# Kernel tuning notes

Hardware: AMD Instinct MI355X
Metric: run time of the kernel (lower is better)

The kernel has to match this reference:

```python
import jax, jax.numpy as jnp
import numpy as np

NUM_NODES = 100000
HIDDEN = 128
OFFSET = 2  # GNNEmbedding.OFFSET


def gcn_conv(x, src, dst, W, b, n):
    # GCNConv: D^{-1/2} (A + I) D^{-1/2} X W + b, with self-loops added
    loops = jnp.arange(n)
    s = jnp.concatenate([src, loops])
    d = jnp.concatenate([dst, loops])
    deg = jax.ops.segment_sum(jnp.ones(s.shape, x.dtype), d, num_segments=n)
    dinv = jax.lax.rsqrt(jnp.maximum(deg, 1e-12))
    norm = dinv[s] * dinv[d]          # [E+n]
    msg = x[s] * norm[:, None]        # [E+n, H]  dominant memory traffic
    agg = jax.ops.segment_sum(msg, d, num_segments=n)
    return agg @ W + b


def setup_inputs():
    key = jax.random.key(0)
    ks = jax.random.split(key, 8)
    E = 1_600_000
    B, S = 16, 2048
    src = jax.random.randint(ks[0], (E,), 0, NUM_NODES)
    dst = jax.random.randint(ks[1], (E,), 0, NUM_NODES)
    ei = jnp.stack([src, dst])
    seq = jax.random.randint(ks[2], (B, S), 0, NUM_NODES)
    specials = jax.random.randint(ks[3], (B, S), -2, 20)
    seq = jnp.where(specials < 0, specials, seq)
    emb = jax.random.normal(ks[4], (NUM_NODES + 2, HIDDEN), jnp.float32) * 0.02
    lim = 1.0 / np.sqrt(HIDDEN)
    W0 = jax.random.uniform(ks[5], (HIDDEN, HIDDEN), jnp.float32, -lim, lim)
    W1 = jax.random.uniform(ks[6], (HIDDEN, HIDDEN), jnp.float32, -lim, lim)
    b0 = jnp.zeros((HIDDEN,), jnp.float32)
    b1 = jnp.zeros((HIDDEN,), jnp.float32)
    return {"emb": emb, "W0": W0, "b0": b0, "W1": W1, "b1": b1,
            "ei": ei, "seq": seq}


def reference(emb, W0, b0, W1, b1, ei, seq):
    src, dst = ei[0], ei[1]
    x = emb[:NUM_NODES]                               # embedding(arange(num_nodes))
    h = jax.nn.relu(gcn_conv(x, src, dst, W0, b0, NUM_NODES))
    z = gcn_conv(h, src, dst, W1, b1, NUM_NODES)      # no act on last GCN layer
    nodes = seq >= 0
    node_idx = jnp.where(nodes, seq, 0)
    spec_idx = jnp.where(nodes, 0, seq + OFFSET + NUM_NODES)
    # embs[nodes] = z[seq[nodes]]; embs[~nodes] = emb[seq+OFFSET+num_nodes]
    embs = jnp.where(nodes[..., None], z[node_idx], emb[spec_idx])
    return embs
```

## Files before the change

kernel.cpp:

```cpp
#include <hip/hip_runtime.h>

#define HDIM 128
#define OFF_SPECIAL 2
#define BSTRIDE 48

typedef __attribute__((ext_vector_type(8))) short bf16x8;
typedef __attribute__((ext_vector_type(4))) float f32x4;

__device__ __forceinline__ float bf2f(unsigned short u) {
    union { unsigned int i; float f; } v;
    v.i = ((unsigned int)u) << 16;
    return v.f;
}
__device__ __forceinline__ unsigned short f2bf(float f) {
    union { float f; unsigned int i; } v;
    v.f = f;
    unsigned int x = v.i;
    x += 0x7FFFu + ((x >> 16) & 1u);
    return (unsigned short)(x >> 16);
}

#define FILL_BLOCKS 1024
#define CAST_BLOCKS 512
#define FLAG_BLOCKS 16

__global__ void k_fill_cast(const int* __restrict__ src, const int* __restrict__ dst,
                            int E, int* __restrict__ cnt, int* __restrict__ adjB,
                            int partN,
                            const float* __restrict__ emb,
                            unsigned short* __restrict__ embbf, int n4,
                            const int* __restrict__ seqp, int P,
                            unsigned char* __restrict__ flag) {
    int tid = threadIdx.x;
    if (blockIdx.x < FILL_BLOCKS) {
        int part = blockIdx.x & 7;
        int blk  = blockIdx.x >> 3;
        int lo = part * partN;
        int hi = lo + partN;
        int nGroups = (E + 3) >> 2;
        int stride = (FILL_BLOCKS >> 3) * 256;
        for (int g = blk * 256 + tid; g < nGroups; g += stride) {
            int4 d4 = ((const int4*)dst)[g];
            int4 s4 = ((const int4*)src)[g];
            int e0 = g * 4;
            int dd[4] = {d4.x, d4.y, d4.z, d4.w};
            int ss[4] = {s4.x, s4.y, s4.z, s4.w};
#pragma unroll
            for (int j = 0; j < 4; ++j) {
                int d = dd[j];
                if (e0 + j < E && d >= lo && d < hi) {
                    int slot = atomicAdd(&cnt[d], 1);
                    if (slot < BSTRIDE) adjB[d * BSTRIDE + slot] = ss[j];
                }
            }
        }
    } else if (blockIdx.x < FILL_BLOCKS + CAST_BLOCKS) {
        int i0 = (blockIdx.x - FILL_BLOCKS) * 256 + tid;
        for (int i = i0; i < n4; i += CAST_BLOCKS * 256) {
            float4 v = ((const float4*)emb)[i];
            ushort4 o;
            o.x = f2bf(v.x); o.y = f2bf(v.y); o.z = f2bf(v.z); o.w = f2bf(v.w);
            ((ushort4*)embbf)[i] = o;
        }
    } else {
        int i0 = (blockIdx.x - FILL_BLOCKS - CAST_BLOCKS) * 256 + tid;
        for (int p = i0; p < P; p += FLAG_BLOCKS * 256) {
            int sv = seqp[p];
            if (sv >= 0) flag[sv] = 1;
        }
    }
}

__global__ void k_dinv(const int* __restrict__ cnt, float* __restrict__ dinv, int N) {
    int i = blockIdx.x * blockDim.x + threadIdx.x;
    if (i < N) dinv[i] = rsqrtf((float)cnt[i] + 1.0f);
}

template <int SPARSE>
__global__ __launch_bounds__(256, 8) void k_pull(
        const unsigned short* __restrict__ x, const int* __restrict__ cnt,
        const int* __restrict__ adjB, const float* __restrict__ dinv,
        unsigned short* __restrict__ agg, int N,
        const unsigned char* __restrict__ flag) {
    int row = blockIdx.x * 4 + (threadIdx.x >> 6);
    if (row >= N) return;
    if (SPARSE && !flag[row]) return;
    int lane = threadIdx.x & 63;
    int d = cnt[row];
    if (d > BSTRIDE) d = BSTRIDE;
    const int* nbr = adjB + row * BSTRIDE;
    float dr = dinv[row];
    unsigned int cix = 2u * (unsigned int)lane;

    float ax, ay;
    {
        float sc = dr * dr;
        unsigned int u = *(const unsigned int*)(x + (size_t)(unsigned)row * HDIM + cix);
        ax = bf2f((unsigned short)u) * sc;
        ay = bf2f((unsigned short)(u >> 16)) * sc;
    }
    int t = 0;
    for (; t + 8 <= d; t += 8) {
        int4 q0 = *(const int4*)(nbr + t);
        int4 q1 = *(const int4*)(nbr + t + 4);
        int s[8] = {q0.x, q0.y, q0.z, q0.w, q1.x, q1.y, q1.z, q1.w};
        float nr[8];
        unsigned int u[8];
#pragma unroll
        for (int i = 0; i < 8; ++i) {
            nr[i] = dinv[s[i]] * dr;
            u[i] = *(const unsigned int*)(x + (size_t)(unsigned)s[i] * HDIM + cix);
        }
#pragma unroll
        for (int i = 0; i < 8; ++i) {
            ax = fmaf(bf2f((unsigned short)u[i]), nr[i], ax);
            ay = fmaf(bf2f((unsigned short)(u[i] >> 16)), nr[i], ay);
        }
    }
    if (t + 4 <= d) {
        int4 q0 = *(const int4*)(nbr + t);
        int s[4] = {q0.x, q0.y, q0.z, q0.w};
        float nr[4];
        unsigned int u[4];
#pragma unroll
        for (int i = 0; i < 4; ++i) {
            nr[i] = dinv[s[i]] * dr;
            u[i] = *(const unsigned int*)(x + (size_t)(unsigned)s[i] * HDIM + cix);
        }
#pragma unroll
        for (int i = 0; i < 4; ++i) {
            ax = fmaf(bf2f((unsigned short)u[i]), nr[i], ax);
            ay = fmaf(bf2f((unsigned short)(u[i] >> 16)), nr[i], ay);
        }
        t += 4;
    }
    for (; t < d; ++t) {
        int s = nbr[t];
        float nr = dinv[s] * dr;
        unsigned int u = *(const unsigned int*)(x + (size_t)(unsigned)s * HDIM + cix);
        ax = fmaf(bf2f((unsigned short)u), nr, ax);
        ay = fmaf(bf2f((unsigned short)(u >> 16)), nr, ay);
    }
    unsigned int pack = (unsigned int)f2bf(ax) | ((unsigned int)f2bf(ay) << 16);
    *(unsigned int*)(agg + (size_t)(unsigned)row * HDIM + cix) = pack;
}

template <int RELU, int SPARSE>
__global__ __launch_bounds__(256) void k_gemm_mfma(
        const unsigned short* __restrict__ A, const float* __restrict__ W,
        const float* __restrict__ bias, unsigned short* __restrict__ out, int N,
        const unsigned char* __restrict__ flag) {
    __shared__ __align__(16) unsigned short Wt[HDIM * 136];
    int tid = threadIdx.x;
    for (int i = tid; i < HDIM * HDIM; i += 256) {
        int k = i >> 7, n = i & 127;
        Wt[n * 136 + k] = f2bf(W[i]);
    }
    int lane = tid & 63;
    int wv = tid >> 6;
    int n15 = lane & 15, q = lane >> 4;
    float bv[8];
#pragma unroll
    for (int ct = 0; ct < 8; ++ct) bv[ct] = bias[ct * 16 + n15];
    __syncthreads();

    int nChunks = (N + 63) / 64;
    for (int c = blockIdx.x; c < nChunks; c += gridDim.x) {
        int row0 = c * 64 + wv * 16;
        if (SPARSE) {
            int frow = row0 + n15;
            int fl = (frow < N) ? flag[frow] : 0;
            if (__ballot(fl != 0) == 0ULL) continue;
        }
        const unsigned short* arow = A + (size_t)(row0 + n15) * HDIM + q * 8;
        bf16x8 a0 = *(const bf16x8*)(arow);
        bf16x8 a1 = *(const bf16x8*)(arow + 32);
        bf16x8 a2 = *(const bf16x8*)(arow + 64);
        bf16x8 a3 = *(const bf16x8*)(arow + 96);
#pragma unroll
        for (int ct = 0; ct < 8; ++ct) {
            const unsigned short* wrow = &Wt[(ct * 16 + n15) * 136 + q * 8];
            f32x4 acc = {0.f, 0.f, 0.f, 0.f};
            acc = __builtin_amdgcn_mfma_f32_16x16x32_bf16(a0, *(const bf16x8*)(wrow),      acc, 0, 0, 0);
            acc = __builtin_amdgcn_mfma_f32_16x16x32_bf16(a1, *(const bf16x8*)(wrow + 32), acc, 0, 0, 0);
            acc = __builtin_amdgcn_mfma_f32_16x16x32_bf16(a2, *(const bf16x8*)(wrow + 64), acc, 0, 0, 0);
            acc = __builtin_amdgcn_mfma_f32_16x16x32_bf16(a3, *(const bf16x8*)(wrow + 96), acc, 0, 0, 0);
#pragma unroll
            for (int r = 0; r < 4; ++r) {
                int row = row0 + q * 4 + r;
                if (row < N && (!SPARSE || flag[row])) {
                    float v = acc[r] + bv[ct];
                    if (RELU) v = fmaxf(v, 0.0f);
                    out[(size_t)row * HDIM + ct * 16 + n15] = f2bf(v);
                }
            }
        }
    }
}

__global__ void k_gather(const int* __restrict__ seq, int P,
                         const unsigned short* __restrict__ z,
                         const float* __restrict__ emb, int N,
                         float* __restrict__ out) {
    int gid = blockIdx.x * blockDim.x + threadIdx.x;
    int p = gid >> 5, c = gid & 31;
    if (p >= P) return;
    int sv = seq[p];
    float4 v;
    if (sv >= 0) {
        uint2 u = *(const uint2*)(z + (size_t)sv * HDIM + c * 4);
        v = make_float4(bf2f((unsigned short)u.x), bf2f((unsigned short)(u.x >> 16)),
                        bf2f((unsigned short)u.y), bf2f((unsigned short)(u.y >> 16)));
    } else {
        v = *(const float4*)(emb + (size_t)(sv + OFF_SPECIAL + N) * HDIM + c * 4);
    }
    *(float4*)(out + (size_t)p * HDIM + c * 4) = v;
}

extern "C" void kernel_launch(void* const* d_in, const int* in_sizes, int n_in,
                              void* d_out, int out_size, void* d_ws, size_t ws_size,
                              hipStream_t stream) {
    const float* emb = (const float*)d_in[0];
    const float* W0  = (const float*)d_in[1];
    const float* b0  = (const float*)d_in[2];
    const float* W1  = (const float*)d_in[3];
    const float* b1  = (const float*)d_in[4];
    const int* ei  = (const int*)d_in[5];
    const int* seq = (const int*)d_in[6];

    int N = in_sizes[0] / HDIM - OFF_SPECIAL;
    int E = in_sizes[5] / 2;
    int P = in_sizes[6];
    const int* srcp = ei;
    const int* dstp = ei + E;

    char* ws = (char*)d_ws;
    size_t off = 0;
    auto alloc = [&](size_t bytes) {
        void* p = ws + off;
        off = (off + bytes + 255) & ~(size_t)255;
        return p;
    };
    unsigned short* aggbf = (unsigned short*)alloc((size_t)N * HDIM * sizeof(unsigned short));
    unsigned short* buf1  = (unsigned short*)alloc((size_t)N * HDIM * sizeof(unsigned short));
    int*   adjB = (int*)alloc((size_t)N * BSTRIDE * sizeof(int));
    int*   cnt  = (int*)alloc((size_t)N * sizeof(int));
    unsigned char* flag = (unsigned char*)alloc((size_t)N);
    float* dinv = (float*)alloc((size_t)N * sizeof(float));

    hipMemsetAsync(cnt, 0, (size_t)((char*)flag - (char*)cnt) + (size_t)N, stream);

    int partN = (N + 7) / 8;
    int n4 = N * HDIM / 4;
    k_fill_cast<<<FILL_BLOCKS + CAST_BLOCKS + FLAG_BLOCKS, 256, 0, stream>>>(
        srcp, dstp, E, cnt, adjB, partN, emb, buf1, n4, seq, P, flag);
    k_dinv<<<(N + 255) / 256, 256, 0, stream>>>(cnt, dinv, N);

    int pullBlocks = (N + 3) / 4;

    k_pull<0><<<pullBlocks, 256, 0, stream>>>(buf1, cnt, adjB, dinv, aggbf, N, nullptr);
    k_gemm_mfma<1, 0><<<640, 256, 0, stream>>>(aggbf, W0, b0, buf1, N, nullptr);

    k_pull<1><<<pullBlocks, 256, 0, stream>>>(buf1, cnt, adjB, dinv, aggbf, N, flag);
    k_gemm_mfma<0, 1><<<640, 256, 0, stream>>>(aggbf, W1, b1, aggbf, N, flag);

    k_gather<<<(P * 32 + 255) / 256, 256, 0, stream>>>(seq, P, aggbf, emb, N,
                                                       (float*)d_out);
}
```

Measured before the change: 325.8 us.

## Build adjacency via atomicExch linked lists then flatten per destination

Replaces the partitioned atomicAdd bucket fill with a single pass over dst that pushes each edge onto a per-node linked list using atomicExch. A follow-up kernel walks each list to fill the fixed-stride adjacency, count and dinv, which also absorbs the separate dinv kernel. This removes the eightfold rescans of the edge arrays and contention on the count atomics. In exchange, the flatten step does serial, dependent random loads per node, and it reuses the aggbf and dinv buffers as scratch space for the list links and heads.

Result: slower. 384.4 us (+18.0%).

```diff
diff --git a/kernel.cpp b/kernel.cpp
--- a/kernel.cpp
+++ b/kernel.cpp
@@ -20,42 +20,38 @@
     return (unsigned short)(x >> 16);
 }
 
-#define FILL_BLOCKS 1024
+#define SCAN_BLOCKS 1024
 #define CAST_BLOCKS 512
 #define FLAG_BLOCKS 16
 
-__global__ void k_fill_cast(const int* __restrict__ src, const int* __restrict__ dst,
-                            int E, int* __restrict__ cnt, int* __restrict__ adjB,
-                            int partN,
+__global__ void k_scan_cast(const int* __restrict__ dst, int E,
+                            int* __restrict__ head, int* __restrict__ nextA,
                             const float* __restrict__ emb,
                             unsigned short* __restrict__ embbf, int n4,
                             const int* __restrict__ seqp, int P,
                             unsigned char* __restrict__ flag) {
     int tid = threadIdx.x;
-    if (blockIdx.x < FILL_BLOCKS) {
-        int part = blockIdx.x & 7;
-        int blk  = blockIdx.x >> 3;
-        int lo = part * partN;
-        int hi = lo + partN;
+    if (blockIdx.x < SCAN_BLOCKS) {
         int nGroups = (E + 3) >> 2;
-        int stride = (FILL_BLOCKS >> 3) * 256;
-        for (int g = blk * 256 + tid; g < nGroups; g += stride) {
+        for (int g = blockIdx.x * 256 + tid; g < nGroups; g += SCAN_BLOCKS * 256) {
             int4 d4 = ((const int4*)dst)[g];
-            int4 s4 = ((const int4*)src)[g];
             int e0 = g * 4;
-            int dd[4] = {d4.x, d4.y, d4.z, d4.w};
-            int ss[4] = {s4.x, s4.y, s4.z, s4.w};
-#pragma unroll
-            for (int j = 0; j < 4; ++j) {
-                int d = dd[j];
-                if (e0 + j < E && d >= lo && d < hi) {
-                    int slot = atomicAdd(&cnt[d], 1);
-                    if (slot < BSTRIDE) adjB[d * BSTRIDE + slot] = ss[j];
-                }
+            if (e0 + 3 < E) {
+                int4 old;
+                old.x = atomicExch(&head[d4.x], e0);
+                old.y = atomicExch(&head[d4.y], e0 + 1);
+                old.z = atomicExch(&head[d4.z], e0 + 2);
+                old.w = atomicExch(&head[d4.w], e0 + 3);
+                *(int4*)(nextA + e0) = old;
+            } else {
+                int dd[4] = {d4.x, d4.y, d4.z, d4.w};
+#pragma unroll
+                for (int j = 0; j < 4; ++j)
+                    if (e0 + j < E) nextA[e0 + j] = atomicExch(&dd[j][head], e0 + j);
             }
         }
-    } else if (blockIdx.x < FILL_BLOCKS + CAST_BLOCKS) {
-        int i0 = (blockIdx.x - FILL_BLOCKS) * 256 + tid;
+    } else if (blockIdx.x < SCAN_BLOCKS + CAST_BLOCKS) {
+        int i0 = (blockIdx.x - SCAN_BLOCKS) * 256 + tid;
         for (int i = i0; i < n4; i += CAST_BLOCKS * 256) {
             float4 v = ((const float4*)emb)[i];
             ushort4 o;
@@ -63,7 +59,7 @@
             ((ushort4*)embbf)[i] = o;
         }
     } else {
-        int i0 = (blockIdx.x - FILL_BLOCKS - CAST_BLOCKS) * 256 + tid;
+        int i0 = (blockIdx.x - SCAN_BLOCKS - CAST_BLOCKS) * 256 + tid;
         for (int p = i0; p < P; p += FLAG_BLOCKS * 256) {
             int sv = seqp[p];
             if (sv >= 0) flag[sv] = 1;
@@ -71,9 +67,23 @@
     }
 }
 
-__global__ void k_dinv(const int* __restrict__ cnt, float* __restrict__ dinv, int N) {
-    int i = blockIdx.x * blockDim.x + threadIdx.x;
-    if (i < N) dinv[i] = rsqrtf((float)cnt[i] + 1.0f);
+__global__ void k_flatten(const int* __restrict__ head, const int* __restrict__ nextA,
+                          const int* __restrict__ src, int* __restrict__ adjB,
+                          int* __restrict__ cnt, float* __restrict__ dinv, int N) {
+    int d = blockIdx.x * 256 + threadIdx.x;
+    if (d >= N) return;
+    int e = head[d];
+    int c = 0;
+    int base = d * BSTRIDE;
+    while (e >= 0) {
+        int s = src[e];
+        int en = nextA[e];
+        if (c < BSTRIDE) adjB[base + c] = s;
+        c++;
+        e = en;
+    }
+    cnt[d] = c;
+    dinv[d] = rsqrtf((float)c + 1.0f);
 }
 
 template <int SPARSE>
@@ -247,14 +257,16 @@
     int*   cnt  = (int*)alloc((size_t)N * sizeof(int));
     unsigned char* flag = (unsigned char*)alloc((size_t)N);
     float* dinv = (float*)alloc((size_t)N * sizeof(float));
-
-    hipMemsetAsync(cnt, 0, (size_t)((char*)flag - (char*)cnt) + (size_t)N, stream);
-
-    int partN = (N + 7) / 8;
+    int* nextA = (int*)aggbf;
+    int* head  = (int*)dinv;
+
+    hipMemsetAsync(head, 0xFF, (size_t)N * sizeof(int), stream);
+    hipMemsetAsync(flag, 0, (size_t)N, stream);
+
     int n4 = N * HDIM / 4;
-    k_fill_cast<<<FILL_BLOCKS + CAST_BLOCKS + FLAG_BLOCKS, 256, 0, stream>>>(
-        srcp, dstp, E, cnt, adjB, partN, emb, buf1, n4, seq, P, flag);
-    k_dinv<<<(N + 255) / 256, 256, 0, stream>>>(cnt, dinv, N);
+    k_scan_cast<<<SCAN_BLOCKS + CAST_BLOCKS + FLAG_BLOCKS, 256, 0, stream>>>(
+        dstp, E, head, nextA, emb, buf1, n4, seq, P, flag);
+    k_flatten<<<(N + 255) / 256, 256, 0, stream>>>(head, nextA, srcp, adjB, cnt, dinv, N);
 
     int pullBlocks = (N + 3) / 4;
 
```
